# Optimization experiments

Measured on AMD Instinct MI355X. Metric: run time of the kernel, lower is better.

Reference implementation:

```python
import jax, jax.numpy as jnp
import numpy as np


def _bilinear_sample(fea, x, y):
    # fea: [B,C,H,W]; x,y: [B,D,HW] pixel coords. grid_sample bilinear, zeros padding, align_corners=True
    B, C, H, W = fea.shape
    x0 = jnp.floor(x)
    y0 = jnp.floor(y)
    wx1 = x - x0
    wy1 = y - y0
    flat = fea.reshape(B, C, H * W)

    def corner(xi, yi, w):
        valid = (xi >= 0) & (xi <= W - 1) & (yi >= 0) & (yi <= H - 1)
        idx = jnp.clip(yi, 0, H - 1).astype(jnp.int32) * W + jnp.clip(xi, 0, W - 1).astype(jnp.int32)
        v = jnp.take_along_axis(flat[:, :, None, :], idx[:, None, :, :], axis=3)  # [B,C,D,HW]
        return v * (w * valid)[:, None]

    return (corner(x0, y0, (1 - wx1) * (1 - wy1)) + corner(x0 + 1, y0, wx1 * (1 - wy1))
            + corner(x0, y0 + 1, (1 - wx1) * wy1) + corner(x0 + 1, y0 + 1, wx1 * wy1))


def _build_proj(p):
    # p: [B,2,4,4] -> 4x4 with top 3x4 = K @ [R|t]
    top = jnp.einsum('bij,bjk->bik', p[:, 1, :3, :3], p[:, 0, :3, :4])
    return p[:, 0].at[:, :3, :4].set(top)


def _forward(depth_values, features, proj_matrices, depth_interval, view_weights, CostNum):
    V = features.shape[0]
    ref_fea = features[0]
    B, C, H, W = ref_fea.shape
    # inverse-depth range sampling (per-pixel, CasMVSNet-style)
    inv_d = 1.0 / depth_values[:, 0]                      # [B,H,W]
    itv = depth_interval[:, 0]                            # [B,H,W]
    low = inv_d - (CostNum / 2.0) * itv
    step = (CostNum * itv) / (CostNum - 1)                # (high-low)/(D-1)
    samp = low[:, None] + jnp.arange(CostNum, dtype=inv_d.dtype)[None, :, None, None] * step[:, None]
    depth = (1.0 / samp).reshape(B, CostNum, H * W)       # back to metric depth [B,D,HW]

    ref_inv = jnp.linalg.inv(_build_proj(proj_matrices[:, 0]))
    ys, xs = jnp.meshgrid(jnp.arange(H, dtype=inv_d.dtype), jnp.arange(W, dtype=inv_d.dtype), indexing='ij')
    xyz = jnp.stack([xs.ravel(), ys.ravel(), jnp.ones(H * W, dtype=inv_d.dtype)], 0)  # [3,HW]

    vol = jnp.zeros((B, 1, CostNum, H, W), inv_d.dtype)
    wsum = jnp.full((B, 1, 1, H, W), 1e-5, inv_d.dtype)
    for i in range(1, V):
        proj = jnp.einsum('bij,bjk->bik', _build_proj(proj_matrices[:, i]), ref_inv)
        rot_xyz = jnp.einsum('bij,jn->bin', proj[:, :3, :3], xyz)                     # [B,3,HW]
        pxyz = rot_xyz[:, :, None, :] * depth[:, None] + proj[:, :3, 3][:, :, None, None]
        gx = pxyz[:, 0] / pxyz[:, 2]
        gy = pxyz[:, 1] / pxyz[:, 2]
        warped = _bilinear_sample(features[i], gx, gy).reshape(B, C, CostNum, H, W)
        wv = (warped * ref_fea[:, :, None]).mean(axis=1, keepdims=True)               # [B,1,D,H,W]
        vw = view_weights[:, i - 1][:, None, None]                                    # [B,1,1,H,W]
        vol = vol + wv * vw
        wsum = wsum + vw
    sim = vol / wsum
    # torch broadcasts [B,1,D,H,W] into the [B,C,D,H,W] buffer -> all C channels equal
    return jnp.broadcast_to(sim, (B, C, CostNum, H, W)).reshape(B, C * CostNum, H, W)


def setup_inputs():
    key = jax.random.key(0)
    ks = jax.random.split(key, 4)
    V, B, C, H, W = 5, 2, 32, 256, 320
    features = jax.random.normal(ks[0], (V, B, C, H, W), jnp.float32)
    depth_values = jax.random.uniform(ks[1], (B, 1, H, W), jnp.float32, minval=0.5, maxval=2.0)
    depth_interval = jax.random.uniform(ks[2], (B, 1, H, W), jnp.float32, minval=0.01, maxval=0.03)
    view_weights = jax.random.uniform(ks[3], (B, V - 1, H, W), jnp.float32, minval=0.1, maxval=1.0)
    K = np.array([[300.0, 0.0, W / 2.0], [0.0, 300.0, H / 2.0], [0.0, 0.0, 1.0]], np.float32)
    proj = np.zeros((B, V, 2, 4, 4), np.float32)
    for v in range(V):
        E = np.eye(4, dtype=np.float32)
        E[0, 3] = 0.1 * v  # camera baseline along x
        proj[:, v, 0] = E
        proj[:, v, 1] = np.eye(4, dtype=np.float32)
        proj[:, v, 1, :3, :3] = K
    return {"depth_values": depth_values, "features": features, "proj_matrices": jnp.asarray(proj),
            "depth_interval": depth_interval, "depth_max": 100, "depth_min": 1, "CostNum": 4,
            "view_weights": view_weights}


def reference(depth_values, features, proj_matrices, depth_interval, depth_max, depth_min, CostNum, view_weights):
    # depth_max/depth_min are unused in the per-pixel sampling path of the original helper
    return _forward(depth_values, features, proj_matrices, depth_interval, view_weights, CostNum)
```

## Files before the change

kernel.cpp:

```cpp
#include <hip/hip_runtime.h>

static constexpr int V  = 5;
static constexpr int B  = 2;
static constexpr int C  = 32;
static constexpr int H  = 256;
static constexpr int W  = 320;
static constexpr int CN = 4;
static constexpr int HW = H * W;
static constexpr int CG = 8;
static constexpr int NG = 4;
static constexpr int XT = W / 64;

static constexpr size_t PARTIAL_FLOATS = (size_t)B * (V - 1) * CN * HW;
static constexpr size_t PARAMS_OFF     = PARTIAL_FLOATS;

static constexpr int FIN_NC = 4;

typedef float f32x2 __attribute__((ext_vector_type(2)));
typedef float f32x4 __attribute__((ext_vector_type(4)));

__device__ __forceinline__ f32x2 ld2(const float* p) {
    f32x2 v;
    __builtin_memcpy(&v, p, sizeof(f32x2));
    return v;
}

__global__ void setup_proj_kernel(const float* __restrict__ pm, float* __restrict__ params) {
    int b = threadIdx.x;
    if (b >= B) return;

    float M[V][16];
    for (int v = 0; v < V; ++v) {
        const float* E  = pm + ((size_t)(b * V + v) * 2 + 0) * 16;
        const float* Km = pm + ((size_t)(b * V + v) * 2 + 1) * 16;
        for (int r = 0; r < 3; ++r)
            for (int c = 0; c < 4; ++c) {
                float s = 0.f;
                for (int k = 0; k < 3; ++k) s += Km[r * 4 + k] * E[k * 4 + c];
                M[v][r * 4 + c] = s;
            }
        for (int c = 0; c < 4; ++c) M[v][12 + c] = E[12 + c];
    }

    float A[9], bb[3];
    for (int r = 0; r < 3; ++r) {
        for (int c = 0; c < 3; ++c) A[r * 3 + c] = M[0][r * 4 + c];
        bb[r] = M[0][r * 4 + 3];
    }
    float det = A[0] * (A[4] * A[8] - A[5] * A[7])
              - A[1] * (A[3] * A[8] - A[5] * A[6])
              + A[2] * (A[3] * A[7] - A[4] * A[6]);
    float id = 1.f / det;
    float Ai[9];
    Ai[0] = (A[4] * A[8] - A[5] * A[7]) * id;
    Ai[1] = (A[2] * A[7] - A[1] * A[8]) * id;
    Ai[2] = (A[1] * A[5] - A[2] * A[4]) * id;
    Ai[3] = (A[5] * A[6] - A[3] * A[8]) * id;
    Ai[4] = (A[0] * A[8] - A[2] * A[6]) * id;
    Ai[5] = (A[2] * A[3] - A[0] * A[5]) * id;
    Ai[6] = (A[3] * A[7] - A[4] * A[6]) * id;
    Ai[7] = (A[1] * A[6] - A[0] * A[7]) * id;
    Ai[8] = (A[0] * A[4] - A[1] * A[3]) * id;
    float bi[3];
    for (int r = 0; r < 3; ++r)
        bi[r] = -(Ai[r * 3 + 0] * bb[0] + Ai[r * 3 + 1] * bb[1] + Ai[r * 3 + 2] * bb[2]);

    float Minv[16];
    for (int r = 0; r < 3; ++r) {
        for (int c = 0; c < 3; ++c) Minv[r * 4 + c] = Ai[r * 3 + c];
        Minv[r * 4 + 3] = bi[r];
    }
    Minv[12] = 0.f; Minv[13] = 0.f; Minv[14] = 0.f; Minv[15] = 1.f;

    for (int v = 1; v < V; ++v) {
        float* dst = params + (size_t)(b * (V - 1) + (v - 1)) * 12;
        for (int r = 0; r < 3; ++r)
            for (int c = 0; c < 4; ++c) {
                float s = 0.f;
                for (int k = 0; k < 4; ++k) s += M[v][r * 4 + k] * Minv[k * 4 + c];
                dst[r * 4 + c] = s;
            }
    }
}

__global__ __launch_bounds__(256) void partial_kernel(
    const float* __restrict__ depth_values,
    const float* __restrict__ features,
    const float* __restrict__ depth_interval,
    const float* __restrict__ view_weights,
    const float* __restrict__ params,
    float* __restrict__ partial)
{
    const int tid = threadIdx.x;
    const int p   = tid & 63;
    const int g   = tid >> 6;

    const int lid = blockIdx.x + XT * (blockIdx.y + H * blockIdx.z);
    const int r   = lid & 7;
    const int q   = lid >> 3;
    const int b   = r >> 2;
    const int iv  = r & 3;
    const int xt  = q % XT;
    const int y   = q / XT;

    const int x   = xt * 64 + p;
    const int pix = y * W + x;

    __shared__ float sp[12];
    __shared__ float sred[NG][CN][64];
    if (tid < 12) sp[tid] = params[(size_t)(b * (V - 1) + iv) * 12 + tid];
    __syncthreads();

    const float invd = 1.f / depth_values[(size_t)b * HW + pix];
    const float itv  = depth_interval[(size_t)b * HW + pix];
    const float low  = invd - (CN * 0.5f) * itv;
    const float step = (CN * itv) / (float)(CN - 1);
    float dep[CN];
#pragma unroll
    for (int k = 0; k < CN; ++k) dep[k] = 1.f / (low + (float)k * step);

    const float* refp = features + ((size_t)b * C + g * CG) * HW + pix;
    float rf[CG];
#pragma unroll
    for (int c = 0; c < CG; ++c) rf[c] = __builtin_nontemporal_load(refp + (size_t)c * HW);

    const float fx = (float)x, fy = (float)y;
    const float rx = sp[0] * fx + sp[1] * fy + sp[2];
    const float ry = sp[4] * fx + sp[5] * fy + sp[6];
    const float rz = sp[8] * fx + sp[9] * fy + sp[10];
    const float tx = sp[3], ty = sp[7], tz = sp[11];

    const float* src = features + ((size_t)((iv + 1) * B + b) * C + g * CG) * HW;
    const float vw = view_weights[((size_t)b * (V - 1) + iv) * HW + pix];
    const float scale = vw * (1.f / (float)C);

    int   ib0[CN], ib1[CN];
    float wA0[CN], wB0[CN], wA1[CN], wB1[CN];
#pragma unroll
    for (int k = 0; k < CN; ++k) {
        const float d  = dep[k];
        const float px = rx * d + tx;
        const float py = ry * d + ty;
        const float pz = rz * d + tz;
        const float iz = 1.f / pz;
        const float gx = px * iz;
        const float gy = py * iz;

        const float x0f = floorf(gx), y0f = floorf(gy);
        const float wx1 = gx - x0f, wy1 = gy - y0f;
        const float wx0 = 1.f - wx1, wy0 = 1.f - wy1;
        const int x0 = (int)x0f, y0 = (int)y0f;
        const int x1 = x0 + 1, y1 = y0 + 1;

        const bool vx0 = (x0 >= 0) && (x0 <= W - 1);
        const bool vx1 = (x1 >= 0) && (x1 <= W - 1);
        const bool vy0 = (y0 >= 0) && (y0 <= H - 1);
        const bool vy1 = (y1 >= 0) && (y1 <= H - 1);

        const int cy0 = min(max(y0, 0), H - 1);
        const int cy1 = min(max(y1, 0), H - 1);
        const int bx  = min(max(x0, 0), W - 2);
        const int s   = x0 - bx;

        const float w00 = wx0 * wy0 * ((vx0 && vy0) ? scale : 0.f);
        const float w10 = wx1 * wy0 * ((vx1 && vy0) ? scale : 0.f);
        const float w01 = wx0 * wy1 * ((vx0 && vy1) ? scale : 0.f);
        const float w11 = wx1 * wy1 * ((vx1 && vy1) ? scale : 0.f);

        wA0[k] = (s == 0) ? w00 : ((s == -1) ? w10 : 0.f);
        wB0[k] = (s == 0) ? w10 : ((s == 1) ? w00 : 0.f);
        wA1[k] = (s == 0) ? w01 : ((s == -1) ? w11 : 0.f);
        wB1[k] = (s == 0) ? w11 : ((s == 1) ? w01 : 0.f);

        ib0[k] = cy0 * W + bx;
        ib1[k] = cy1 * W + bx;
    }

    float vol[CN] = {0.f, 0.f, 0.f, 0.f};
#pragma unroll
    for (int cc = 0; cc < CG; cc += 4) {
        f32x2 P0[4][CN], P1[4][CN];
#pragma unroll
        for (int c = 0; c < 4; ++c) {
            const float* fc = src + (size_t)(cc + c) * HW;
#pragma unroll
            for (int k = 0; k < CN; ++k) {
                P0[c][k] = ld2(fc + ib0[k]);
                P1[c][k] = ld2(fc + ib1[k]);
            }
        }
#pragma unroll
        for (int c = 0; c < 4; ++c) {
            const float rfc = rf[cc + c];
#pragma unroll
            for (int k = 0; k < CN; ++k) {
                float t = wA0[k] * P0[c][k].x;
                t = fmaf(wB0[k], P0[c][k].y, t);
                t = fmaf(wA1[k], P1[c][k].x, t);
                t = fmaf(wB1[k], P1[c][k].y, t);
                vol[k] = fmaf(rfc, t, vol[k]);
            }
        }
    }

#pragma unroll
    for (int k = 0; k < CN; ++k) sred[g][k][p] = vol[k];
    __syncthreads();

    {
        const int k = g;
        float s = sred[0][k][p] + sred[1][k][p] + sred[2][k][p] + sred[3][k][p];
        float* dst = partial + ((size_t)(b * (V - 1) + iv) * CN + k) * HW + pix;
        *dst = s;
    }
}

__global__ __launch_bounds__(256) void finalize_kernel(
    const float* __restrict__ partial,
    const float* __restrict__ view_weights,
    float* __restrict__ out)
{
    const int t   = blockIdx.x * 256 + threadIdx.x;
    const int idx = t * 4;
    const int b   = idx / HW;
    const int pix = idx - b * HW;
    const int c0  = blockIdx.y * FIN_NC;

    f32x4 wsum = {1e-5f, 1e-5f, 1e-5f, 1e-5f};
#pragma unroll
    for (int i = 0; i < V - 1; ++i) {
        f32x4 vw = *(const f32x4*)(view_weights + ((size_t)b * (V - 1) + i) * HW + pix);
        wsum += vw;
    }
    const f32x4 iw = {1.f / wsum.x, 1.f / wsum.y, 1.f / wsum.z, 1.f / wsum.w};

    f32x4 sim[CN];
#pragma unroll
    for (int k = 0; k < CN; ++k) {
        f32x4 s = {0.f, 0.f, 0.f, 0.f};
#pragma unroll
        for (int i = 0; i < V - 1; ++i)
            s += *(const f32x4*)(partial + ((size_t)(b * (V - 1) + i) * CN + k) * HW + pix);
        sim[k] = s * iw;
    }

    float* op = out + (size_t)b * C * CN * HW + pix;
#pragma unroll
    for (int ci = 0; ci < FIN_NC; ++ci) {
        const int c = c0 + ci;
#pragma unroll
        for (int k = 0; k < CN; ++k)
            __builtin_nontemporal_store(sim[k], (f32x4*)(op + (size_t)(c * CN + k) * HW));
    }
}

extern "C" void kernel_launch(void* const* d_in, const int* in_sizes, int n_in,
                              void* d_out, int out_size, void* d_ws, size_t ws_size,
                              hipStream_t stream) {
    const float* depth_values   = (const float*)d_in[0];
    const float* features       = (const float*)d_in[1];
    const float* proj_matrices  = (const float*)d_in[2];
    const float* depth_interval = (const float*)d_in[3];
    const float* view_weights   = (const float*)d_in[7];
    float* out     = (float*)d_out;
    float* partial = (float*)d_ws;
    float* params  = (float*)d_ws + PARAMS_OFF;

    setup_proj_kernel<<<1, B, 0, stream>>>(proj_matrices, params);

    dim3 grid1(XT, H, B * (V - 1));
    partial_kernel<<<grid1, 256, 0, stream>>>(depth_values, features, depth_interval,
                                              view_weights, params, partial);

    dim3 grid2(B * HW / 1024, C / FIN_NC);
    finalize_kernel<<<grid2, 256, 0, stream>>>(partial, view_weights, out);
}
```

Baseline: 292.4 us.

## Fuse per-view partial and finalize kernels into one view-looping kernel

Merges the per-view partial kernel and the finalize kernel into a single kernel in which each block loops over all source views and accumulates the correlation volume in registers. The weight sum is normalised in-block and the result is broadcast to all C channel planes through LDS with vectorized stores. This drops the partial workspace write and read and one kernel launch, and adds a swizzled block-to-tile mapping. In exchange each block now does four times the gather work, so there are four times fewer blocks to hide latency with, and the output stores are no longer nontemporal.

```diff
diff --git a/kernel.cpp b/kernel.cpp
--- a/kernel.cpp
+++ b/kernel.cpp
@@ -10,11 +10,9 @@
 static constexpr int CG = 8;
 static constexpr int NG = 4;
 static constexpr int XT = W / 64;
-
-static constexpr size_t PARTIAL_FLOATS = (size_t)B * (V - 1) * CN * HW;
-static constexpr size_t PARAMS_OFF     = PARTIAL_FLOATS;
-
-static constexpr int FIN_NC = 4;
+static constexpr int NBLK = XT * H * B;
+
+static constexpr size_t PARAMS_OFF = 0;
 
 typedef float f32x2 __attribute__((ext_vector_type(2)));
 typedef float f32x4 __attribute__((ext_vector_type(4)));
@@ -83,32 +81,32 @@
     }
 }
 
-__global__ __launch_bounds__(256) void partial_kernel(
+__global__ __launch_bounds__(256) void fused_kernel(
     const float* __restrict__ depth_values,
     const float* __restrict__ features,
     const float* __restrict__ depth_interval,
     const float* __restrict__ view_weights,
     const float* __restrict__ params,
-    float* __restrict__ partial)
+    float* __restrict__ out)
 {
     const int tid = threadIdx.x;
     const int p   = tid & 63;
     const int g   = tid >> 6;
 
-    const int lid = blockIdx.x + XT * (blockIdx.y + H * blockIdx.z);
-    const int r   = lid & 7;
-    const int q   = lid >> 3;
-    const int b   = r >> 2;
-    const int iv  = r & 3;
-    const int xt  = q % XT;
-    const int y   = q / XT;
+    const int d  = blockIdx.x;
+    const int l  = (d & 7) * (NBLK / 8) + (d >> 3);
+    const int xt = l % XT;
+    const int r2 = l / XT;
+    const int y  = r2 & (H - 1);
+    const int b  = r2 >> 8;
 
     const int x   = xt * 64 + p;
     const int pix = y * W + x;
 
-    __shared__ float sp[12];
+    __shared__ float sp4[48];
     __shared__ float sred[NG][CN][64];
-    if (tid < 12) sp[tid] = params[(size_t)(b * (V - 1) + iv) * 12 + tid];
+    __shared__ float sim_lds[CN][64];
+    if (tid < 48) sp4[tid] = params[(size_t)b * 48 + tid];
     __syncthreads();
 
     const float invd = 1.f / depth_values[(size_t)b * HW + pix];
@@ -125,132 +123,114 @@
     for (int c = 0; c < CG; ++c) rf[c] = __builtin_nontemporal_load(refp + (size_t)c * HW);
 
     const float fx = (float)x, fy = (float)y;
-    const float rx = sp[0] * fx + sp[1] * fy + sp[2];
-    const float ry = sp[4] * fx + sp[5] * fy + sp[6];
-    const float rz = sp[8] * fx + sp[9] * fy + sp[10];
-    const float tx = sp[3], ty = sp[7], tz = sp[11];
-
-    const float* src = features + ((size_t)((iv + 1) * B + b) * C + g * CG) * HW;
-    const float vw = view_weights[((size_t)b * (V - 1) + iv) * HW + pix];
-    const float scale = vw * (1.f / (float)C);
-
-    int   ib0[CN], ib1[CN];
-    float wA0[CN], wB0[CN], wA1[CN], wB1[CN];
-#pragma unroll
-    for (int k = 0; k < CN; ++k) {
-        const float d  = dep[k];
-        const float px = rx * d + tx;
-        const float py = ry * d + ty;
-        const float pz = rz * d + tz;
-        const float iz = 1.f / pz;
-        const float gx = px * iz;
-        const float gy = py * iz;
-
-        const float x0f = floorf(gx), y0f = floorf(gy);
-        const float wx1 = gx - x0f, wy1 = gy - y0f;
-        const float wx0 = 1.f - wx1, wy0 = 1.f - wy1;
-        const int x0 = (int)x0f, y0 = (int)y0f;
-        const int x1 = x0 + 1, y1 = y0 + 1;
-
-        const bool vx0 = (x0 >= 0) && (x0 <= W - 1);
-        const bool vx1 = (x1 >= 0) && (x1 <= W - 1);
-        const bool vy0 = (y0 >= 0) && (y0 <= H - 1);
-        const bool vy1 = (y1 >= 0) && (y1 <= H - 1);
-
-        const int cy0 = min(max(y0, 0), H - 1);
-        const int cy1 = min(max(y1, 0), H - 1);
-        const int bx  = min(max(x0, 0), W - 2);
-        const int s   = x0 - bx;
-
-        const float w00 = wx0 * wy0 * ((vx0 && vy0) ? scale : 0.f);
-        const float w10 = wx1 * wy0 * ((vx1 && vy0) ? scale : 0.f);
-        const float w01 = wx0 * wy1 * ((vx0 && vy1) ? scale : 0.f);
-        const float w11 = wx1 * wy1 * ((vx1 && vy1) ? scale : 0.f);
-
-        wA0[k] = (s == 0) ? w00 : ((s == -1) ? w10 : 0.f);
-        wB0[k] = (s == 0) ? w10 : ((s == 1) ? w00 : 0.f);
-        wA1[k] = (s == 0) ? w01 : ((s == -1) ? w11 : 0.f);
-        wB1[k] = (s == 0) ? w11 : ((s == 1) ? w01 : 0.f);
-
-        ib0[k] = cy0 * W + bx;
-        ib1[k] = cy1 * W + bx;
-    }
-
-    float vol[CN] = {0.f, 0.f, 0.f, 0.f};
-#pragma unroll
-    for (int cc = 0; cc < CG; cc += 4) {
-        f32x2 P0[4][CN], P1[4][CN];
-#pragma unroll
-        for (int c = 0; c < 4; ++c) {
-            const float* fc = src + (size_t)(cc + c) * HW;
-#pragma unroll
-            for (int k = 0; k < CN; ++k) {
-                P0[c][k] = ld2(fc + ib0[k]);
-                P1[c][k] = ld2(fc + ib1[k]);
-            }
+
+    float volsum[CN] = {0.f, 0.f, 0.f, 0.f};
+    float wsum = 1e-5f;
+
+    for (int iv = 0; iv < V - 1; ++iv) {
+        const float* spv = &sp4[iv * 12];
+        const float rx = spv[0] * fx + spv[1] * fy + spv[2];
+        const float ry = spv[4] * fx + spv[5] * fy + spv[6];
+        const float rz = spv[8] * fx + spv[9] * fy + spv[10];
+        const float tx = spv[3], ty = spv[7], tz = spv[11];
+
+        const float vw = view_weights[((size_t)b * (V - 1) + iv) * HW + pix];
+        wsum += vw;
+        const float scale = vw * (1.f / (float)C);
+
+        const float* src = features + ((size_t)((iv + 1) * B + b) * C + g * CG) * HW;
+
+        int   ib0[CN], ib1[CN];
+        float wA0[CN], wB0[CN], wA1[CN], wB1[CN];
+#pragma unroll
+        for (int k = 0; k < CN; ++k) {
+            const float dd = dep[k];
+            const float px = rx * dd + tx;
+            const float py = ry * dd + ty;
+            const float pz = rz * dd + tz;
+            const float iz = 1.f / pz;
+            const float gx = px * iz;
+            const float gy = py * iz;
+
+            const float x0f = floorf(gx), y0f = floorf(gy);
+            const float wx1 = gx - x0f, wy1 = gy - y0f;
+            const float wx0 = 1.f - wx1, wy0 = 1.f - wy1;
+            const int x0 = (int)x0f, y0 = (int)y0f;
+            const int x1 = x0 + 1, y1 = y0 + 1;
+
+            const bool vx0 = (x0 >= 0) && (x0 <= W - 1);
+            const bool vx1 = (x1 >= 0) && (x1 <= W - 1);
+            const bool vy0 = (y0 >= 0) && (y0 <= H - 1);
+            const bool vy1 = (y1 >= 0) && (y1 <= H - 1);
+
+            const int cy0 = min(max(y0, 0), H - 1);
+            const int cy1 = min(max(y1, 0), H - 1);
+            const int bx  = min(max(x0, 0), W - 2);
+            const int s   = x0 - bx;
+
+            const float w00 = wx0 * wy0 * ((vx0 && vy0) ? scale : 0.f);
+            const float w10 = wx1 * wy0 * ((vx1 && vy0) ? scale : 0.f);
+            const float w01 = wx0 * wy1 * ((vx0 && vy1) ? scale : 0.f);
+            const float w11 = wx1 * wy1 * ((vx1 && vy1) ? scale : 0.f);
+
+            wA0[k] = (s == 0) ? w00 : ((s == -1) ? w10 : 0.f);
+            wB0[k] = (s == 0) ? w10 : ((s == 1) ? w00 : 0.f);
+            wA1[k] = (s == 0) ? w01 : ((s == -1) ? w11 : 0.f);
+            wB1[k] = (s == 0) ? w11 : ((s == 1) ? w01 : 0.f);
+
+            ib0[k] = cy0 * W + bx;
+            ib1[k] = cy1 * W + bx;
         }
-#pragma unroll
-        for (int c = 0; c < 4; ++c) {
-            const float rfc = rf[cc + c];
-#pragma unroll
-            for (int k = 0; k < CN; ++k) {
-                float t = wA0[k] * P0[c][k].x;
-                t = fmaf(wB0[k], P0[c][k].y, t);
-                t = fmaf(wA1[k], P1[c][k].x, t);
-                t = fmaf(wB1[k], P1[c][k].y, t);
-                vol[k] = fmaf(rfc, t, vol[k]);
+
+#pragma unroll
+        for (int cc = 0; cc < CG; cc += 4) {
+            f32x2 P0[4][CN], P1[4][CN];
+#pragma unroll
+            for (int c = 0; c < 4; ++c) {
+                const float* fc = src + (size_t)(cc + c) * HW;
+#pragma unroll
+                for (int k = 0; k < CN; ++k) {
+                    P0[c][k] = ld2(fc + ib0[k]);
+                    P1[c][k] = ld2(fc + ib1[k]);
+                }
+            }
+#pragma unroll
+            for (int c = 0; c < 4; ++c) {
+                const float rfc = rf[cc + c];
+#pragma unroll
+                for (int k = 0; k < CN; ++k) {
+                    float t = wA0[k] * P0[c][k].x;
+                    t = fmaf(wB0[k], P0[c][k].y, t);
+                    t = fmaf(wA1[k], P1[c][k].x, t);
+                    t = fmaf(wB1[k], P1[c][k].y, t);
+                    volsum[k] = fmaf(rfc, t, volsum[k]);
+                }
             }
         }
     }
 
 #pragma unroll
-    for (int k = 0; k < CN; ++k) sred[g][k][p] = vol[k];
+    for (int k = 0; k < CN; ++k) sred[g][k][p] = volsum[k];
     __syncthreads();
 
     {
         const int k = g;
-        float s = sred[0][k][p] + sred[1][k][p] + sred[2][k][p] + sred[3][k][p];
-        float* dst = partial + ((size_t)(b * (V - 1) + iv) * CN + k) * HW + pix;
-        *dst = s;
-    }
-}
-
-__global__ __launch_bounds__(256) void finalize_kernel(
-    const float* __restrict__ partial,
-    const float* __restrict__ view_weights,
-    float* __restrict__ out)
-{
-    const int t   = blockIdx.x * 256 + threadIdx.x;
-    const int idx = t * 4;
-    const int b   = idx / HW;
-    const int pix = idx - b * HW;
-    const int c0  = blockIdx.y * FIN_NC;
-
-    f32x4 wsum = {1e-5f, 1e-5f, 1e-5f, 1e-5f};
-#pragma unroll
-    for (int i = 0; i < V - 1; ++i) {
-        f32x4 vw = *(const f32x4*)(view_weights + ((size_t)b * (V - 1) + i) * HW + pix);
-        wsum += vw;
-    }
-    const f32x4 iw = {1.f / wsum.x, 1.f / wsum.y, 1.f / wsum.z, 1.f / wsum.w};
-
-    f32x4 sim[CN];
-#pragma unroll
-    for (int k = 0; k < CN; ++k) {
-        f32x4 s = {0.f, 0.f, 0.f, 0.f};
-#pragma unroll
-        for (int i = 0; i < V - 1; ++i)
-            s += *(const f32x4*)(partial + ((size_t)(b * (V - 1) + i) * CN + k) * HW + pix);
-        sim[k] = s * iw;
-    }
-
-    float* op = out + (size_t)b * C * CN * HW + pix;
-#pragma unroll
-    for (int ci = 0; ci < FIN_NC; ++ci) {
-        const int c = c0 + ci;
-#pragma unroll
-        for (int k = 0; k < CN; ++k)
-            __builtin_nontemporal_store(sim[k], (f32x4*)(op + (size_t)(c * CN + k) * HW));
+        const float s = sred[0][k][p] + sred[1][k][p] + sred[2][k][p] + sred[3][k][p];
+        sim_lds[k][p] = s * (1.f / wsum);
+    }
+    __syncthreads();
+
+    {
+        const int quad = tid & 15;
+        const int pc   = tid >> 4;
+        float* op = out + (size_t)b * C * CN * HW + y * W + xt * 64 + quad * 4;
+#pragma unroll
+        for (int j = 0; j < 8; ++j) {
+            const int plane = pc * 8 + j;
+            const int k     = plane & 3;
+            const f32x4 v   = *(const f32x4*)&sim_lds[k][quad * 4];
+            *(f32x4*)(op + (size_t)plane * HW) = v;
+        }
     }
 }
 
@@ -262,16 +242,11 @@
     const float* proj_matrices  = (const float*)d_in[2];
     const float* depth_interval = (const float*)d_in[3];
     const float* view_weights   = (const float*)d_in[7];
-    float* out     = (float*)d_out;
-    float* partial = (float*)d_ws;
-    float* params  = (float*)d_ws + PARAMS_OFF;
+    float* out    = (float*)d_out;
+    float* params = (float*)d_ws + PARAMS_OFF;
 
     setup_proj_kernel<<<1, B, 0, stream>>>(proj_matrices, params);
 
-    dim3 grid1(XT, H, B * (V - 1));
-    partial_kernel<<<grid1, 256, 0, stream>>>(depth_values, features, depth_interval,
-                                              view_weights, params, partial);
-
-    dim3 grid2(B * HW / 1024, C / FIN_NC);
-    finalize_kernel<<<grid2, 256, 0, stream>>>(partial, view_weights, out);
-}
+    fused_kernel<<<NBLK, 256, 0, stream>>>(depth_values, features, depth_interval,
+                                           view_weights, params, out);
+}
```

Measured after the change: 284.8 us. -2.6%, faster.
